# Kernel tuning notes

Measured on AMD Instinct MI355X. Metric: run time of the kernel, lower is better.

## Reference

```python
import jax, jax.numpy as jnp
import numpy as np

B, N, OBS, H, A, R = 16384, 32, 64, 64, 16, 2


def setup_inputs() -> dict:
    key = jax.random.key(0)
    ks = jax.random.split(key, 11)
    s = lambda fan_in: 1.0 / np.sqrt(fan_in)
    return {
        "obs": jax.random.normal(ks[0], (B, N, OBS), dtype=jnp.float32),
        "enc_w": jax.random.uniform(ks[1], (OBS, H), jnp.float32, -s(OBS), s(OBS)),
        "enc_b": jax.random.uniform(ks[2], (H,), jnp.float32, -s(OBS), s(OBS)),
        "comm_w": jax.random.uniform(ks[3], (R, 2 * H, H), jnp.float32, -s(2 * H), s(2 * H)),
        "comm_b": jax.random.uniform(ks[4], (R, H), jnp.float32, -s(2 * H), s(2 * H)),
        "out_w1": jax.random.uniform(ks[5], (H, H), jnp.float32, -s(H), s(H)),
        "out_b1": jax.random.uniform(ks[6], (H,), jnp.float32, -s(H), s(H)),
        "out_w2": jax.random.uniform(ks[7], (H, A), jnp.float32, -s(H), s(H)),
        "out_b2": jax.random.uniform(ks[8], (A,), jnp.float32, -s(H), s(H)),
        "available_actions": jax.random.randint(ks[9], (B, N, A), 0, 2, dtype=jnp.int32),
    }


def reference(obs, enc_w, enc_b, comm_w, comm_b, out_w1, out_b1, out_w2, out_b2, available_actions):
    # obs: [B, N, OBS]
    h = jax.nn.relu(jnp.einsum("bno,oh->bnh", obs, enc_w) + enc_b)  # [B,N,H]
    n_agents = h.shape[1]
    for r in range(comm_w.shape[0]):  # fixed small number of comm rounds
        # mean over other agents == (sum - self) / (n-1); fuses the per-agent loop
        msg = (jnp.sum(h, axis=1, keepdims=True) - h) / (n_agents - 1)
        combined = jnp.concatenate([h, msg], axis=-1)  # [B,N,2H]
        h = jax.nn.relu(jnp.einsum("bnk,kh->bnh", combined, comm_w[r]) + comm_b[r])
    hid = jax.nn.relu(jnp.einsum("bnh,hk->bnk", h, out_w1) + out_b1)
    q = jnp.einsum("bnh,ha->bna", hid, out_w2) + out_b2  # [B,N,A]
    q = jnp.where(available_actions == 0, jnp.float32(-1e10), q)
    return q
```

## Files before the change

kernel.cpp:

```cpp
#include <hip/hip_runtime.h>

#define NBATCH 16384
#define NAG 32
#define DOBS 64
#define DH 64
#define DA 16
#define LSTRIDE 72
#define WSLOT 2432
#define NLDSF 32
#define NWAVES 4


typedef __attribute__((ext_vector_type(8))) short bf16x8;
typedef __attribute__((ext_vector_type(4))) float f32x4;

__device__ __forceinline__ short f2bf(float f) {
  return (short)(__float_as_uint(f) >> 16);
}
__device__ __forceinline__ short f2bf_rne(float f) {
  unsigned u = __float_as_uint(f);
  return (short)((u + 0x7fffu + ((u >> 16) & 1u)) >> 16);
}

__global__ void build_frags(const float* __restrict__ enc_w, const float* __restrict__ comm_w,
                            const float* __restrict__ out_w1, const float* __restrict__ out_w2,
                            short* __restrict__ wf) {
  int e = blockIdx.x * blockDim.x + threadIdx.x;
  if (e >= 50 * 512) return;
  int f = e >> 9;
  int lane = (e >> 3) & 63;
  int j = e & 7;
  int quad = lane >> 4, col = lane & 15;
  float val;
  if (f < 8) {
    int kk = (f >> 2) & 1, nn = f & 3;
    int k = kk * 32 + quad * 8 + j, n = nn * 16 + col;
    val = enc_w[k * DH + n];
  } else if (f < 24) {
    int g = f - 8; int r = g >> 3, kk = (g >> 2) & 1, nn = g & 3;
    int k = kk * 32 + quad * 8 + j, n = nn * 16 + col;
    const float* W = comm_w + r * (2 * DH * DH);
    val = W[k * DH + n] - W[(DH + k) * DH + n] * (1.0f / 31.0f);
  } else if (f < 40) {
    int g = f - 24; int r = g >> 3, kk = (g >> 2) & 1, nn = g & 3;
    int k = kk * 32 + quad * 8 + j, n = nn * 16 + col;
    const float* W = comm_w + r * (2 * DH * DH);
    val = W[(DH + k) * DH + n] * (1.0f / 31.0f);
  } else if (f < 48) {
    int g = f - 40; int kk = (g >> 2) & 1, nn = g & 3;
    int k = kk * 32 + quad * 8 + j, n = nn * 16 + col;
    val = out_w1[k * DH + n];
  } else {
    int kk = f - 48;
    int k = kk * 32 + quad * 8 + j;
    val = out_w2[k * DA + col];
  }
  wf[e] = f2bf_rne(val);
}

template<bool WITH_T, bool WITH_S>
__device__ __forceinline__ void stage_h(const f32x4 (&acc)[2][4], const float (&t)[4],
                                        short* hb, short* sb, int quad, int col) {
#pragma unroll
  for (int nn = 0; nn < 4; nn++) {
    float s = 0.f;
#pragma unroll
    for (int m2 = 0; m2 < 2; m2++) {
#pragma unroll
      for (int r = 0; r < 4; r++) {
        float v = acc[m2][nn][r];
        if constexpr (WITH_T) v += t[nn];
        v = fmaxf(v, 0.f);
        hb[(m2 * 16 + quad * 4 + r) * LSTRIDE + nn * 16 + col] = f2bf(v);
        if constexpr (WITH_S) s += v;
      }
    }
    if constexpr (WITH_S) {
      s += __shfl_xor(s, 16, 64);
      s += __shfl_xor(s, 32, 64);
      sb[nn * 16 + col] = f2bf(s);
    }
  }
}

__device__ __forceinline__ void read_afrags(bf16x8 (&ah)[2][2], const short* hb, int quad, int col) {
#pragma unroll
  for (int m2 = 0; m2 < 2; m2++)
#pragma unroll
    for (int kk = 0; kk < 2; kk++)
      ah[m2][kk] = *(const bf16x8*)(hb + (m2 * 16 + col) * LSTRIDE + kk * 32 + quad * 8);
}

__device__ __forceinline__ void read_sfrags(bf16x8 (&as)[2], const short* sb, int quad, int col) {
  const bf16x8 z = {0, 0, 0, 0, 0, 0, 0, 0};
#pragma unroll
  for (int kk = 0; kk < 2; kk++) {
    bf16x8 v = *(const bf16x8*)(sb + kk * 32 + quad * 8);
    as[kk] = (col == 0) ? v : z;
  }
}

__device__ __forceinline__ void issue_obs(const float* __restrict__ obs, int b,
                                          int quad, int col, f32x4 (&pf)[8]) {
#pragma unroll
  for (int m2 = 0; m2 < 2; m2++)
#pragma unroll
    for (int kk = 0; kk < 2; kk++) {
      const float* p = obs + ((b * NAG + m2 * 16 + col) * DOBS + kk * 32 + quad * 8);
      pf[(m2 * 2 + kk) * 2 + 0] = *(const f32x4*)p;
      pf[(m2 * 2 + kk) * 2 + 1] = *(const f32x4*)(p + 4);
    }
}

__device__ __forceinline__ void issue_avail(const int* __restrict__ avail, int b,
                                            int quad, int col, int (&pav)[8]) {
#pragma unroll
  for (int m2 = 0; m2 < 2; m2++)
#pragma unroll
    for (int r = 0; r < 4; r++) {
      int row = m2 * 16 + quad * 4 + r;
      pav[m2 * 4 + r] = avail[(b * NAG + row) * DA + col];
    }
}

__device__ __forceinline__ bf16x8 wfrag(const bf16x8* __restrict__ wf,
                                        const short* lw, int f, int lane) {
  return (f < 8 || f >= 40) ? wf[f * 64 + lane]
                            : *(const bf16x8*)(lw + (f - 8) * 512 + lane * 8);
}

__global__ void __launch_bounds__(256, 2) commnet_main(
    const float* __restrict__ obs,
    const float* __restrict__ enc_b,
    const float* __restrict__ comm_b,
    const float* __restrict__ out_b1,
    const float* __restrict__ out_b2,
    const int* __restrict__ avail,
    const short* __restrict__ wf_raw,
    float* __restrict__ out) {
  __shared__ short lds_w[NLDSF * 512];
  __shared__ short hbuf[NWAVES * WSLOT];
  const int tid = threadIdx.x;
  const int wave = tid >> 6;
  const int lane = tid & 63;
  const int quad = lane >> 4, col = lane & 15;
  short* hb = hbuf + wave * WSLOT;
  short* sb = hb + 2304;
  const bf16x8* wf = (const bf16x8*)wf_raw;

  for (int f = 8 + wave; f < 40; f += NWAVES)
    *(bf16x8*)(lds_w + (f - 8) * 512 + lane * 8) = wf[f * 64 + lane];

  int b = blockIdx.x * NWAVES + wave;
  const int wstep = 3072;

  f32x4 pf[8];
  int pav[8];
  issue_obs(obs, b, quad, col, pf);
  issue_avail(avail, b, quad, col, pav);

  float eb[4], cbb[2][4], ob1[4];
#pragma unroll
  for (int nn = 0; nn < 4; nn++) {
    eb[nn] = enc_b[nn * 16 + col];
    cbb[0][nn] = comm_b[nn * 16 + col];
    cbb[1][nn] = comm_b[DH + nn * 16 + col];
    ob1[nn] = out_b1[nn * 16 + col];
  }
  float ob2 = out_b2[col];

  __syncthreads();

#pragma unroll 1
  for (;;) {
    const int bnx = b + wstep;
    const int bn = (bnx < NBATCH) ? bnx : 0;

    bf16x8 aob[2][2];
#pragma unroll
    for (int m2 = 0; m2 < 2; m2++)
#pragma unroll
      for (int kk = 0; kk < 2; kk++) {
        f32x4 x0 = pf[(m2 * 2 + kk) * 2 + 0];
        f32x4 x1 = pf[(m2 * 2 + kk) * 2 + 1];
        bf16x8 a;
        a[0] = f2bf(x0[0]); a[1] = f2bf(x0[1]); a[2] = f2bf(x0[2]); a[3] = f2bf(x0[3]);
        a[4] = f2bf(x1[0]); a[5] = f2bf(x1[1]); a[6] = f2bf(x1[2]); a[7] = f2bf(x1[3]);
        aob[m2][kk] = a;
      }
    issue_obs(obs, bn, quad, col, pf);

    f32x4 acc[2][4];
#pragma unroll
    for (int nn = 0; nn < 4; nn++) {
      f32x4 c; c[0] = c[1] = c[2] = c[3] = eb[nn];
      acc[0][nn] = c; acc[1][nn] = c;
    }
#pragma unroll
    for (int kk = 0; kk < 2; kk++) {
#pragma unroll
      for (int nn = 0; nn < 4; nn++) {
        bf16x8 w = wfrag(wf, lds_w, kk * 4 + nn, lane);
        acc[0][nn] = __builtin_amdgcn_mfma_f32_16x16x32_bf16(aob[0][kk], w, acc[0][nn], 0, 0, 0);
        acc[1][nn] = __builtin_amdgcn_mfma_f32_16x16x32_bf16(aob[1][kk], w, acc[1][nn], 0, 0, 0);
      }
    }
    float tz[4] = {0.f, 0.f, 0.f, 0.f};
    stage_h<false, true>(acc, tz, hb, sb, quad, col);
    bf16x8 ah[2][2]; read_afrags(ah, hb, quad, col);
    bf16x8 as[2];    read_sfrags(as, sb, quad, col);

#pragma unroll
    for (int r = 0; r < 2; r++) {
      f32x4 aS[4];
#pragma unroll
      for (int nn = 0; nn < 4; nn++) { f32x4 z; z[0] = z[1] = z[2] = z[3] = 0.f; aS[nn] = z; }
#pragma unroll
      for (int kk = 0; kk < 2; kk++)
#pragma unroll
        for (int nn = 0; nn < 4; nn++) {
          bf16x8 vv = wfrag(wf, lds_w, 24 + r * 8 + kk * 4 + nn, lane);
          aS[nn] = __builtin_amdgcn_mfma_f32_16x16x32_bf16(as[kk], vv, aS[nn], 0, 0, 0);
        }
      float t[4];
#pragma unroll
      for (int nn = 0; nn < 4; nn++) t[nn] = __shfl(aS[nn][0], col, 64);

      f32x4 a2[2][4];
#pragma unroll
      for (int nn = 0; nn < 4; nn++) {
        f32x4 c; c[0] = c[1] = c[2] = c[3] = cbb[r][nn];
        a2[0][nn] = c; a2[1][nn] = c;
      }
#pragma unroll
      for (int kk = 0; kk < 2; kk++)
#pragma unroll
        for (int nn = 0; nn < 4; nn++) {
          bf16x8 we = wfrag(wf, lds_w, 8 + r * 8 + kk * 4 + nn, lane);
          a2[0][nn] = __builtin_amdgcn_mfma_f32_16x16x32_bf16(ah[0][kk], we, a2[0][nn], 0, 0, 0);
          a2[1][nn] = __builtin_amdgcn_mfma_f32_16x16x32_bf16(ah[1][kk], we, a2[1][nn], 0, 0, 0);
        }
      if (r == 0) {
        stage_h<true, true>(a2, t, hb, sb, quad, col);
        read_afrags(ah, hb, quad, col);
        read_sfrags(as, sb, quad, col);
      } else {
        stage_h<true, false>(a2, t, hb, sb, quad, col);
        read_afrags(ah, hb, quad, col);
      }
    }

    f32x4 a3[2][4];
#pragma unroll
    for (int nn = 0; nn < 4; nn++) {
      f32x4 c; c[0] = c[1] = c[2] = c[3] = ob1[nn];
      a3[0][nn] = c; a3[1][nn] = c;
    }
#pragma unroll
    for (int kk = 0; kk < 2; kk++)
#pragma unroll
      for (int nn = 0; nn < 4; nn++) {
        bf16x8 w = wfrag(wf, lds_w, 40 + kk * 4 + nn, lane);
        a3[0][nn] = __builtin_amdgcn_mfma_f32_16x16x32_bf16(ah[0][kk], w, a3[0][nn], 0, 0, 0);
        a3[1][nn] = __builtin_amdgcn_mfma_f32_16x16x32_bf16(ah[1][kk], w, a3[1][nn], 0, 0, 0);
      }
    stage_h<false, false>(a3, tz, hb, sb, quad, col);
    read_afrags(ah, hb, quad, col);

    f32x4 a4[2];
    {
      f32x4 c; c[0] = c[1] = c[2] = c[3] = ob2;
      a4[0] = c; a4[1] = c;
    }
#pragma unroll
    for (int kk = 0; kk < 2; kk++) {
      bf16x8 w = wfrag(wf, lds_w, 48 + kk, lane);
      a4[0] = __builtin_amdgcn_mfma_f32_16x16x32_bf16(ah[0][kk], w, a4[0], 0, 0, 0);
      a4[1] = __builtin_amdgcn_mfma_f32_16x16x32_bf16(ah[1][kk], w, a4[1], 0, 0, 0);
    }
#pragma unroll
    for (int m2 = 0; m2 < 2; m2++) {
#pragma unroll
      for (int r = 0; r < 4; r++) {
        int row = m2 * 16 + quad * 4 + r;
        int idx = (b * NAG + row) * DA + col;
        float q = a4[m2][r];
        out[idx] = (pav[m2 * 4 + r] == 0) ? -1e10f : q;
      }
    }
    issue_avail(avail, bn, quad, col, pav);

    if (bnx >= NBATCH) break;
    b = bnx;
  }
}

extern "C" void kernel_launch(void* const* d_in, const int* in_sizes, int n_in,
                              void* d_out, int out_size, void* d_ws, size_t ws_size,
                              hipStream_t stream) {
  const float* obs    = (const float*)d_in[0];
  const float* enc_w  = (const float*)d_in[1];
  const float* enc_b  = (const float*)d_in[2];
  const float* comm_w = (const float*)d_in[3];
  const float* comm_b = (const float*)d_in[4];
  const float* out_w1 = (const float*)d_in[5];
  const float* out_b1 = (const float*)d_in[6];
  const float* out_w2 = (const float*)d_in[7];
  const float* out_b2 = (const float*)d_in[8];
  const int*   avail  = (const int*)d_in[9];
  short* wf = (short*)d_ws;

  build_frags<<<100, 256, 0, stream>>>(enc_w, comm_w, out_w1, out_w2, wf);
  commnet_main<<<768, 256, 0, stream>>>(obs, enc_b, comm_b, out_b1, out_b2, avail, wf,
                                        (float*)d_out);
}
```

Baseline: 251.6 us.

## Split each batch across a wave pair with shared agent-sum exchange

Each batch element's 32 agents are now handled by two waves of 16 rows each, not one wave. The per-wave column sums go to shared memory as fp32 partials, and after a block barrier each wave adds its partner's partial. Blocks grow to 512 threads and out_w1 fragments also move into LDS. The aim is to halve per-wave register and MFMA work and raise parallelism, at the cost of two block-wide __syncthreads per iteration.

```diff
diff --git a/kernel.cpp b/kernel.cpp
--- a/kernel.cpp
+++ b/kernel.cpp
@@ -6,9 +6,9 @@
 #define DH 64
 #define DA 16
 #define LSTRIDE 72
-#define WSLOT 2432
-#define NLDSF 32
-#define NWAVES 4
+#define HSLOT (16 * LSTRIDE)
+#define NLDSF 40
+#define BWAVES 8
 
 
 typedef __attribute__((ext_vector_type(8))) short bf16x8;
@@ -59,77 +59,75 @@
 }
 
 template<bool WITH_T, bool WITH_S>
-__device__ __forceinline__ void stage_h(const f32x4 (&acc)[2][4], const float (&t)[4],
-                                        short* hb, short* sb, int quad, int col) {
+__device__ __forceinline__ void stage_h(const f32x4 (&acc)[4], const float (&t)[4],
+                                        short* hb, float* sp, int quad, int col) {
 #pragma unroll
   for (int nn = 0; nn < 4; nn++) {
     float s = 0.f;
 #pragma unroll
-    for (int m2 = 0; m2 < 2; m2++) {
-#pragma unroll
-      for (int r = 0; r < 4; r++) {
-        float v = acc[m2][nn][r];
-        if constexpr (WITH_T) v += t[nn];
-        v = fmaxf(v, 0.f);
-        hb[(m2 * 16 + quad * 4 + r) * LSTRIDE + nn * 16 + col] = f2bf(v);
-        if constexpr (WITH_S) s += v;
-      }
+    for (int r = 0; r < 4; r++) {
+      float v = acc[nn][r];
+      if constexpr (WITH_T) v += t[nn];
+      v = fmaxf(v, 0.f);
+      hb[(quad * 4 + r) * LSTRIDE + nn * 16 + col] = f2bf(v);
+      if constexpr (WITH_S) s += v;
     }
     if constexpr (WITH_S) {
       s += __shfl_xor(s, 16, 64);
       s += __shfl_xor(s, 32, 64);
-      sb[nn * 16 + col] = f2bf(s);
-    }
-  }
-}
-
-__device__ __forceinline__ void read_afrags(bf16x8 (&ah)[2][2], const short* hb, int quad, int col) {
-#pragma unroll
-  for (int m2 = 0; m2 < 2; m2++)
-#pragma unroll
-    for (int kk = 0; kk < 2; kk++)
-      ah[m2][kk] = *(const bf16x8*)(hb + (m2 * 16 + col) * LSTRIDE + kk * 32 + quad * 8);
-}
-
-__device__ __forceinline__ void read_sfrags(bf16x8 (&as)[2], const short* sb, int quad, int col) {
+      sp[nn * 16 + col] = s;
+    }
+  }
+}
+
+__device__ __forceinline__ void read_afrags(bf16x8 (&ah)[2], const short* hb, int quad, int col) {
+#pragma unroll
+  for (int kk = 0; kk < 2; kk++)
+    ah[kk] = *(const bf16x8*)(hb + col * LSTRIDE + kk * 32 + quad * 8);
+}
+
+__device__ __forceinline__ void read_sfrags(bf16x8 (&as)[2], const float* spA, const float* spB,
+                                            int quad, int col) {
   const bf16x8 z = {0, 0, 0, 0, 0, 0, 0, 0};
 #pragma unroll
   for (int kk = 0; kk < 2; kk++) {
-    bf16x8 v = *(const bf16x8*)(sb + kk * 32 + quad * 8);
+    const float* pa = spA + kk * 32 + quad * 8;
+    const float* pb = spB + kk * 32 + quad * 8;
+    f32x4 a0 = *(const f32x4*)pa, a1 = *(const f32x4*)(pa + 4);
+    f32x4 b0 = *(const f32x4*)pb, b1 = *(const f32x4*)(pb + 4);
+    bf16x8 v;
+    v[0] = f2bf(a0[0] + b0[0]); v[1] = f2bf(a0[1] + b0[1]);
+    v[2] = f2bf(a0[2] + b0[2]); v[3] = f2bf(a0[3] + b0[3]);
+    v[4] = f2bf(a1[0] + b1[0]); v[5] = f2bf(a1[1] + b1[1]);
+    v[6] = f2bf(a1[2] + b1[2]); v[7] = f2bf(a1[3] + b1[3]);
     as[kk] = (col == 0) ? v : z;
   }
 }
 
-__device__ __forceinline__ void issue_obs(const float* __restrict__ obs, int b,
-                                          int quad, int col, f32x4 (&pf)[8]) {
-#pragma unroll
-  for (int m2 = 0; m2 < 2; m2++)
-#pragma unroll
-    for (int kk = 0; kk < 2; kk++) {
-      const float* p = obs + ((b * NAG + m2 * 16 + col) * DOBS + kk * 32 + quad * 8);
-      pf[(m2 * 2 + kk) * 2 + 0] = *(const f32x4*)p;
-      pf[(m2 * 2 + kk) * 2 + 1] = *(const f32x4*)(p + 4);
-    }
-}
-
-__device__ __forceinline__ void issue_avail(const int* __restrict__ avail, int b,
-                                            int quad, int col, int (&pav)[8]) {
-#pragma unroll
-  for (int m2 = 0; m2 < 2; m2++)
-#pragma unroll
-    for (int r = 0; r < 4; r++) {
-      int row = m2 * 16 + quad * 4 + r;
-      pav[m2 * 4 + r] = avail[(b * NAG + row) * DA + col];
-    }
+__device__ __forceinline__ void issue_obs(const float* __restrict__ obs, int b, int hr,
+                                          int quad, int col, f32x4 (&pf)[4]) {
+#pragma unroll
+  for (int kk = 0; kk < 2; kk++) {
+    const float* p = obs + ((b * NAG + hr + col) * DOBS + kk * 32 + quad * 8);
+    pf[kk * 2 + 0] = *(const f32x4*)p;
+    pf[kk * 2 + 1] = *(const f32x4*)(p + 4);
+  }
+}
+
+__device__ __forceinline__ void issue_avail(const int* __restrict__ avail, int b, int hr,
+                                            int quad, int col, int (&pav)[4]) {
+#pragma unroll
+  for (int r = 0; r < 4; r++)
+    pav[r] = avail[(b * NAG + hr + quad * 4 + r) * DA + col];
 }
 
 __device__ __forceinline__ bf16x8 wfrag(const bf16x8* __restrict__ wf,
                                         const short* lw, int f, int lane) {
-  return (f < 8 || f >= 40) ? wf[f * 64 + lane]
+  return (f < 8 || f >= 48) ? wf[f * 64 + lane]
                             : *(const bf16x8*)(lw + (f - 8) * 512 + lane * 8);
 }
 
-__global__ void __launch_bounds__(256, 2) commnet_main(
+__global__ void __launch_bounds__(512, 2) commnet_main(
     const float* __restrict__ obs,
     const float* __restrict__ enc_b,
     const float* __restrict__ comm_b,
@@ -139,25 +137,27 @@
     const short* __restrict__ wf_raw,
     float* __restrict__ out) {
   __shared__ short lds_w[NLDSF * 512];
-  __shared__ short hbuf[NWAVES * WSLOT];
+  __shared__ short hbuf[BWAVES * HSLOT];
+  __shared__ float sbuf[2][4][2][64];
   const int tid = threadIdx.x;
   const int wave = tid >> 6;
   const int lane = tid & 63;
   const int quad = lane >> 4, col = lane & 15;
-  short* hb = hbuf + wave * WSLOT;
-  short* sb = hb + 2304;
+  const int pair = wave >> 1, half = wave & 1;
+  const int hr = half * 16;
+  short* hb = hbuf + wave * HSLOT;
   const bf16x8* wf = (const bf16x8*)wf_raw;
 
-  for (int f = 8 + wave; f < 40; f += NWAVES)
+  for (int f = 8 + wave; f < 48; f += BWAVES)
     *(bf16x8*)(lds_w + (f - 8) * 512 + lane * 8) = wf[f * 64 + lane];
 
-  int b = blockIdx.x * NWAVES + wave;
-  const int wstep = 3072;
-
-  f32x4 pf[8];
-  int pav[8];
-  issue_obs(obs, b, quad, col, pf);
-  issue_avail(avail, b, quad, col, pav);
+  int b = blockIdx.x * 4 + pair;
+  const int wstep = 2048;
+
+  f32x4 pf[4];
+  int pav[4];
+  issue_obs(obs, b, hr, quad, col, pf);
+  issue_avail(avail, b, hr, quad, col, pav);
 
   float eb[4], cbb[2][4], ob1[4];
 #pragma unroll
@@ -176,39 +176,36 @@
     const int bnx = b + wstep;
     const int bn = (bnx < NBATCH) ? bnx : 0;
 
-    bf16x8 aob[2][2];
-#pragma unroll
-    for (int m2 = 0; m2 < 2; m2++)
-#pragma unroll
-      for (int kk = 0; kk < 2; kk++) {
-        f32x4 x0 = pf[(m2 * 2 + kk) * 2 + 0];
-        f32x4 x1 = pf[(m2 * 2 + kk) * 2 + 1];
-        bf16x8 a;
-        a[0] = f2bf(x0[0]); a[1] = f2bf(x0[1]); a[2] = f2bf(x0[2]); a[3] = f2bf(x0[3]);
-        a[4] = f2bf(x1[0]); a[5] = f2bf(x1[1]); a[6] = f2bf(x1[2]); a[7] = f2bf(x1[3]);
-        aob[m2][kk] = a;
-      }
-    issue_obs(obs, bn, quad, col, pf);
-
-    f32x4 acc[2][4];
+    bf16x8 aob[2];
+#pragma unroll
+    for (int kk = 0; kk < 2; kk++) {
+      f32x4 x0 = pf[kk * 2 + 0];
+      f32x4 x1 = pf[kk * 2 + 1];
+      bf16x8 a;
+      a[0] = f2bf(x0[0]); a[1] = f2bf(x0[1]); a[2] = f2bf(x0[2]); a[3] = f2bf(x0[3]);
+      a[4] = f2bf(x1[0]); a[5] = f2bf(x1[1]); a[6] = f2bf(x1[2]); a[7] = f2bf(x1[3]);
+      aob[kk] = a;
+    }
+    issue_obs(obs, bn, hr, quad, col, pf);
+
+    f32x4 acc[4];
 #pragma unroll
     for (int nn = 0; nn < 4; nn++) {
       f32x4 c; c[0] = c[1] = c[2] = c[3] = eb[nn];
-      acc[0][nn] = c; acc[1][nn] = c;
-    }
-#pragma unroll
-    for (int kk = 0; kk < 2; kk++) {
+      acc[nn] = c;
+    }
+#pragma unroll
+    for (int kk = 0; kk < 2; kk++)
 #pragma unroll
       for (int nn = 0; nn < 4; nn++) {
         bf16x8 w = wfrag(wf, lds_w, kk * 4 + nn, lane);
-        acc[0][nn] = __builtin_amdgcn_mfma_f32_16x16x32_bf16(aob[0][kk], w, acc[0][nn], 0, 0, 0);
-        acc[1][nn] = __builtin_amdgcn_mfma_f32_16x16x32_bf16(aob[1][kk], w, acc[1][nn], 0, 0, 0);
+        acc[nn] = __builtin_amdgcn_mfma_f32_16x16x32_bf16(aob[kk], w, acc[nn], 0, 0, 0);
       }
-    }
     float tz[4] = {0.f, 0.f, 0.f, 0.f};
-    stage_h<false, true>(acc, tz, hb, sb, quad, col);
-    bf16x8 ah[2][2]; read_afrags(ah, hb, quad, col);
-    bf16x8 as[2];    read_sfrags(as, sb, quad, col);
+    stage_h<false, true>(acc, tz, hb, &sbuf[0][pair][half][0], quad, col);
+    __syncthreads();
+    bf16x8 ah[2]; read_afrags(ah, hb, quad, col);
+    bf16x8 as[2]; read_sfrags(as, &sbuf[0][pair][0][0], &sbuf[0][pair][1][0], quad, col);
 
 #pragma unroll
     for (int r = 0; r < 2; r++) {
@@ -226,69 +223,60 @@
 #pragma unroll
       for (int nn = 0; nn < 4; nn++) t[nn] = __shfl(aS[nn][0], col, 64);
 
-      f32x4 a2[2][4];
+      f32x4 a2[4];
 #pragma unroll
       for (int nn = 0; nn < 4; nn++) {
         f32x4 c; c[0] = c[1] = c[2] = c[3] = cbb[r][nn];
-        a2[0][nn] = c; a2[1][nn] = c;
+        a2[nn] = c;
       }
 #pragma unroll
       for (int kk = 0; kk < 2; kk++)
 #pragma unroll
         for (int nn = 0; nn < 4; nn++) {
           bf16x8 we = wfrag(wf, lds_w, 8 + r * 8 + kk * 4 + nn, lane);
-          a2[0][nn] = __builtin_amdgcn_mfma_f32_16x16x32_bf16(ah[0][kk], we, a2[0][nn], 0, 0, 0);
-          a2[1][nn] = __builtin_amdgcn_mfma_f32_16x16x32_bf16(ah[1][kk], we, a2[1][nn], 0, 0, 0);
+          a2[nn] = __builtin_amdgcn_mfma_f32_16x16x32_bf16(ah[kk], we, a2[nn], 0, 0, 0);
         }
       if (r == 0) {
-        stage_h<true, true>(a2, t, hb, sb, quad, col);
+        stage_h<true, true>(a2, t, hb, &sbuf[1][pair][half][0], quad, col);
+        __syncthreads();
         read_afrags(ah, hb, quad, col);
-        read_sfrags(as, sb, quad, col);
+        read_sfrags(as, &sbuf[1][pair][0][0], &sbuf[1][pair][1][0], quad, col);
       } else {
-        stage_h<true, false>(a2, t, hb, sb, quad, col);
+        stage_h<true, false>(a2, t, hb, nullptr, quad, col);
         read_afrags(ah, hb, quad, col);
       }
     }
 
-    f32x4 a3[2][4];
+    f32x4 a3[4];
 #pragma unroll
     for (int nn = 0; nn < 4; nn++) {
       f32x4 c; c[0] = c[1] = c[2] = c[3] = ob1[nn];
-      a3[0][nn] = c; a3[1][nn] = c;
+      a3[nn] = c;
     }
 #pragma unroll
     for (int kk = 0; kk < 2; kk++)
 #pragma unroll
       for (int nn = 0; nn < 4; nn++) {
         bf16x8 w = wfrag(wf, lds_w, 40 + kk * 4 + nn, lane);
-        a3[0][nn] = __builtin_amdgcn_mfma_f32_16x16x32_bf16(ah[0][kk], w, a3[0][nn], 0, 0, 0);
-        a3[1][nn] = __builtin_amdgcn_mfma_f32_16x16x32_bf16(ah[1][kk], w, a3[1][nn], 0, 0, 0);
+        a3[nn] = __builtin_amdgcn_mfma_f32_16x16x32_bf16(ah[kk], w, a3[nn], 0, 0, 0);
       }
-    stage_h<false, false>(a3, tz, hb, sb, quad, col);
+    stage_h<false, false>(a3, tz, hb, nullptr, quad, col);
     read_afrags(ah, hb, quad, col);
 
-    f32x4 a4[2];
-    {
-      f32x4 c; c[0] = c[1] = c[2] = c[3] = ob2;
-      a4[0] = c; a4[1] = c;
-    }
+    f32x4 a4;
+    a4[0] = a4[1] = a4[2] = a4[3] = ob2;
 #pragma unroll
     for (int kk = 0; kk < 2; kk++) {
       bf16x8 w = wfrag(wf, lds_w, 48 + kk, lane);
-      a4[0] = __builtin_amdgcn_mfma_f32_16x16x32_bf16(ah[0][kk], w, a4[0], 0, 0, 0);
-      a4[1] = __builtin_amdgcn_mfma_f32_16x16x32_bf16(ah[1][kk], w, a4[1], 0, 0, 0);
-    }
-#pragma unroll
-    for (int m2 = 0; m2 < 2; m2++) {
-#pragma unroll
-      for (int r = 0; r < 4; r++) {
-        int row = m2 * 16 + quad * 4 + r;
-        int idx = (b * NAG + row) * DA + col;
-        float q = a4[m2][r];
-        out[idx] = (pav[m2 * 4 + r] == 0) ? -1e10f : q;
-      }
-    }
-    issue_avail(avail, bn, quad, col, pav);
+      a4 = __builtin_amdgcn_mfma_f32_16x16x32_bf16(ah[kk], w, a4, 0, 0, 0);
+    }
+#pragma unroll
+    for (int r = 0; r < 4; r++) {
+      int row = hr + quad * 4 + r;
+      int idx = (b * NAG + row) * DA + col;
+      out[idx] = (pav[r] == 0) ? -1e10f : a4[r];
+    }
+    issue_avail(avail, bn, hr, quad, col, pav);
 
     if (bnx >= NBATCH) break;
     b = bnx;
@@ -311,6 +299,6 @@
   short* wf = (short*)d_ws;
 
   build_frags<<<100, 256, 0, stream>>>(enc_w, comm_w, out_w1, out_w2, wf);
-  commnet_main<<<768, 256, 0, stream>>>(obs, enc_b, comm_b, out_b1, out_b2, avail, wf,
+  commnet_main<<<512, 512, 0, stream>>>(obs, enc_b, comm_b, out_b1, out_b2, avail, wf,
                                         (float*)d_out);
 }
```

Result: no change. 247.7 us (-1.5%).
